# Kernel tuning notes

Measured on AMD Instinct MI355X. Metric: run time of the kernel, lower is better.

## Reference

```python
import jax, jax.numpy as jnp
import numpy as np

B, N, M, D, K = 64, 1024, 1024, 200, 80


def setup_inputs() -> dict:
    key = jax.random.key(0)
    ks = jax.random.split(key, 7)
    return {
        "sentence_rep": jax.random.normal(ks[0], (B, N, D), dtype=jnp.float32),
        "comment_rep": jax.random.normal(ks[1], (B, M, D), dtype=jnp.float32),
        "Wl": jax.random.uniform(ks[2], (D, D), dtype=jnp.float32),
        "Wc": jax.random.uniform(ks[3], (K, D), dtype=jnp.float32),
        "Ws": jax.random.uniform(ks[4], (K, D), dtype=jnp.float32),
        "whs": jax.random.uniform(ks[5], (1, K), dtype=jnp.float32),
        "whc": jax.random.uniform(ks[6], (1, K), dtype=jnp.float32),
    }


def reference(sentence_rep, comment_rep, Wl, Wc, Ws, whs, whc):
    # affinity: L[b,m,n] = tanh((comment @ Wl) @ sent^T)
    L = jnp.tanh(jnp.einsum("bmd,de,bne->bmn", comment_rep, Wl, sentence_rep))
    # projected reps: Ws @ sent^T -> [B,K,N]; Wc @ comment^T -> [B,K,M]
    WsS = jnp.einsum("kd,bnd->bkn", Ws, sentence_rep)
    WcC = jnp.einsum("kd,bmd->bkm", Wc, comment_rep)
    Hs = jnp.tanh(WsS + jnp.einsum("bkm,bmn->bkn", WcC, L))  # [B,K,N]
    Hc = jnp.tanh(WcC + jnp.einsum("bkn,bmn->bkm", WsS, L))  # [B,K,M]
    # NOTE: original uses F.softmax with no dim on a 3D tensor -> legacy dim=0 (batch axis)
    As = jax.nn.softmax(jnp.einsum("ok,bkn->bon", whs, Hs), axis=0)  # [B,1,N]
    Ac = jax.nn.softmax(jnp.einsum("ok,bkm->bom", whc, Hc), axis=0)  # [B,1,M]
    co_s = jnp.einsum("bnd,bon->bd", sentence_rep, As)  # [B,D]
    co_c = jnp.einsum("bmd,bom->bd", comment_rep, Ac)   # [B,D]
    return jnp.concatenate([co_s, co_c], axis=1)  # [B, 2D]
```

## Files before the change

### kernel.cpp

```cpp
#include <hip/hip_runtime.h>
#include <cmath>

constexpr int CB = 64;
constexpr int CN = 1024;
constexpr int CM = 1024;
constexpr int CD = 200;
constexpr int CK = 80;

__global__ __launch_bounds__(256) void k_transpose(const float* __restrict__ Wl,
                                                   float* __restrict__ WlT) {
  int idx = blockIdx.x * 256 + threadIdx.x;
  if (idx < CD * CD) {
    int d = idx / CD, e = idx - d * CD;
    WlT[e * CD + d] = Wl[idx];
  }
}

__global__ __launch_bounds__(256) void k_rowrow(
    const float* __restrict__ A, long sA,
    const float* __restrict__ Bm, long sB,
    float* __restrict__ C, long sC, int ldc, int I, int J)
{
  const int bz = blockIdx.z;
  A  += (size_t)bz * sA;
  Bm += (size_t)bz * sB;
  C  += (size_t)bz * sC;
  const int i0 = blockIdx.x * 64, j0 = blockIdx.y * 64;
  __shared__ float As[2][16][68];
  __shared__ float Bs[2][16][68];
  const int tid = threadIdx.x;
  const int tx = tid & 15, ty = tid >> 4;
  const int lr = tid >> 2, ld4 = (tid & 3) << 2;
  float acc[4][4] = {};
  for (int ci = 0; ci < 13; ++ci) {
    const int dc = ci * 16;
    const int buf = ci & 1;
    float4 va = make_float4(0.f, 0.f, 0.f, 0.f), vb = va;
    const int gd = dc + ld4;
    if (gd < CD) {
      const int gi = i0 + lr;
      if (gi < I) va = *(const float4*)(A + (size_t)gi * CD + gd);
      const int gj = j0 + lr;
      if (gj < J) vb = *(const float4*)(Bm + (size_t)gj * CD + gd);
    }
    As[buf][ld4 + 0][lr] = va.x; As[buf][ld4 + 1][lr] = va.y;
    As[buf][ld4 + 2][lr] = va.z; As[buf][ld4 + 3][lr] = va.w;
    Bs[buf][ld4 + 0][lr] = vb.x; Bs[buf][ld4 + 1][lr] = vb.y;
    Bs[buf][ld4 + 2][lr] = vb.z; Bs[buf][ld4 + 3][lr] = vb.w;
    __syncthreads();
    #pragma unroll
    for (int dd = 0; dd < 16; ++dd) {
      float4 av = *(const float4*)&As[buf][dd][ty * 4];
      float4 bv = *(const float4*)&Bs[buf][dd][tx * 4];
      acc[0][0] += av.x * bv.x; acc[0][1] += av.x * bv.y; acc[0][2] += av.x * bv.z; acc[0][3] += av.x * bv.w;
      acc[1][0] += av.y * bv.x; acc[1][1] += av.y * bv.y; acc[1][2] += av.y * bv.z; acc[1][3] += av.y * bv.w;
      acc[2][0] += av.z * bv.x; acc[2][1] += av.z * bv.y; acc[2][2] += av.z * bv.z; acc[2][3] += av.z * bv.w;
      acc[3][0] += av.w * bv.x; acc[3][1] += av.w * bv.y; acc[3][2] += av.w * bv.z; acc[3][3] += av.w * bv.w;
    }
  }
  #pragma unroll
  for (int ri = 0; ri < 4; ++ri) {
    const int gi = i0 + ty * 4 + ri;
    const int gj = j0 + tx * 4;
    if (gi < I && gj < J) {
      float4 v; v.x = acc[ri][0]; v.y = acc[ri][1]; v.z = acc[ri][2]; v.w = acc[ri][3];
      *(float4*)(C + (size_t)gi * ldc + gj) = v;
    }
  }
}

__global__ __launch_bounds__(256) void k_fused(
    const float* __restrict__ Arows,
    const float* __restrict__ Brows,
    const float* __restrict__ W,
    float* __restrict__ Out)
{
  const int bz = blockIdx.y;
  Arows += (size_t)bz * (CM * CD);
  Brows += (size_t)bz * (CM * CD);
  W     += (size_t)bz * (CK * 1024);
  Out   += (size_t)bz * (CK * 1024);
  const int j0 = blockIdx.x * 32;
  __shared__ float As[2][16][68];
  __shared__ float Bs[2][16][36];
  __shared__ float Xs[64][36];
  __shared__ float Wt[64][81];
  const int tid = threadIdx.x;
  const int tx8 = tid & 7, ty2 = tid >> 3;
  const int jt = tid & 15, kt = tid >> 4;
  const int lr = tid >> 2, ld4 = (tid & 3) << 2;
  float tacc[5][2] = {};
  for (int it = 0; it < 16; ++it) {
    const int i0 = it * 64;
    float4 wv[5];
    #pragma unroll
    for (int rp = 0; rp < 5; ++rp) {
      const int idx4 = rp * 256 + tid;
      wv[rp] = *(const float4*)(W + (size_t)(idx4 >> 4) * 1024 + i0 + ((idx4 & 15) << 2));
    }
    float xacc[2][4] = {};
    for (int ci = 0; ci < 13; ++ci) {
      const int dc = ci * 16;
      const int buf = ci & 1;
      float4 va = make_float4(0.f, 0.f, 0.f, 0.f), vb = va;
      const int gd = dc + ld4;
      if (gd < CD) {
        va = *(const float4*)(Arows + (size_t)(i0 + lr) * CD + gd);
        if (tid < 128) vb = *(const float4*)(Brows + (size_t)(j0 + lr) * CD + gd);
      }
      As[buf][ld4 + 0][lr] = va.x; As[buf][ld4 + 1][lr] = va.y;
      As[buf][ld4 + 2][lr] = va.z; As[buf][ld4 + 3][lr] = va.w;
      if (tid < 128) {
        Bs[buf][ld4 + 0][lr] = vb.x; Bs[buf][ld4 + 1][lr] = vb.y;
        Bs[buf][ld4 + 2][lr] = vb.z; Bs[buf][ld4 + 3][lr] = vb.w;
      }
      __syncthreads();
      #pragma unroll
      for (int dd = 0; dd < 16; ++dd) {
        float2 av = *(const float2*)&As[buf][dd][ty2 * 2];
        float4 bv = *(const float4*)&Bs[buf][dd][tx8 * 4];
        xacc[0][0] += av.x * bv.x; xacc[0][1] += av.x * bv.y;
        xacc[0][2] += av.x * bv.z; xacc[0][3] += av.x * bv.w;
        xacc[1][0] += av.y * bv.x; xacc[1][1] += av.y * bv.y;
        xacc[1][2] += av.y * bv.z; xacc[1][3] += av.y * bv.w;
      }
    }
    #pragma unroll
    for (int r = 0; r < 2; ++r) {
      float4 v;
      v.x = tanhf(xacc[r][0]); v.y = tanhf(xacc[r][1]);
      v.z = tanhf(xacc[r][2]); v.w = tanhf(xacc[r][3]);
      *(float4*)&Xs[ty2 * 2 + r][tx8 * 4] = v;
    }
    #pragma unroll
    for (int rp = 0; rp < 5; ++rp) {
      const int idx4 = rp * 256 + tid;
      const int k = idx4 >> 4, i4 = (idx4 & 15) << 2;
      Wt[i4 + 0][k] = wv[rp].x; Wt[i4 + 1][k] = wv[rp].y;
      Wt[i4 + 2][k] = wv[rp].z; Wt[i4 + 3][k] = wv[rp].w;
    }
    __syncthreads();
    #pragma unroll 8
    for (int i = 0; i < 64; ++i) {
      float2 xv = *(const float2*)&Xs[i][jt * 2];
      #pragma unroll
      for (int c = 0; c < 5; ++c) {
        float w = Wt[i][kt * 5 + c];
        tacc[c][0] += w * xv.x;
        tacc[c][1] += w * xv.y;
      }
    }
  }
  #pragma unroll
  for (int c = 0; c < 5; ++c) {
    const int k = kt * 5 + c;
    float2 v; v.x = tacc[c][0]; v.y = tacc[c][1];
    *(float2*)(Out + (size_t)k * 1024 + j0 + jt * 2) = v;
  }
}

__global__ __launch_bounds__(256) void k_logits(
    const float* __restrict__ WsS, const float* __restrict__ T1, const float* __restrict__ whs,
    const float* __restrict__ WcC, const float* __restrict__ T2, const float* __restrict__ whc,
    float* __restrict__ z)
{
  const int side = blockIdx.z, b = blockIdx.y;
  const int n = blockIdx.x * 256 + threadIdx.x;
  const float* P  = side ? WcC : WsS;
  const float* T  = side ? T2 : T1;
  const float* wh = side ? whc : whs;
  const size_t base = (size_t)b * CK * 1024 + n;
  float acc = 0.f;
  #pragma unroll 8
  for (int k = 0; k < CK; ++k)
    acc += wh[k] * tanhf(P[base + (size_t)k * 1024] + T[base + (size_t)k * 1024]);
  z[((size_t)side * CB + b) * 1024 + n] = acc;
}

__global__ __launch_bounds__(256) void k_softmax(const float* __restrict__ z,
                                                 float* __restrict__ a) {
  const int idx = blockIdx.x * 256 + threadIdx.x;
  if (idx >= 2 * 1024) return;
  const int side = idx >> 10, n = idx & 1023;
  const float* zc = z + (size_t)side * CB * 1024 + n;
  float mx = -1e30f;
  for (int b = 0; b < CB; ++b) mx = fmaxf(mx, zc[(size_t)b * 1024]);
  float s = 0.f;
  for (int b = 0; b < CB; ++b) s += expf(zc[(size_t)b * 1024] - mx);
  const float inv = 1.0f / s;
  float* ac = a + (size_t)side * CB * 1024 + n;
  for (int b = 0; b < CB; ++b) ac[(size_t)b * 1024] = expf(zc[(size_t)b * 1024] - mx) * inv;
}

__global__ __launch_bounds__(256) void k_wsum(
    const float* __restrict__ sent, const float* __restrict__ comm,
    const float* __restrict__ a, float* __restrict__ partial)
{
  const int t = blockIdx.x, b = blockIdx.y, side = blockIdx.z;
  const int d = threadIdx.x;
  if (d >= CD) return;
  const float* rep = side ? comm : sent;
  const float* aw = a + ((size_t)side * CB + b) * 1024;
  float acc = 0.f;
  const int n0 = t * 128;
  #pragma unroll 4
  for (int n = n0; n < n0 + 128; ++n)
    acc += rep[((size_t)b * 1024 + n) * CD + d] * aw[n];
  partial[(((size_t)side * CB + b) * 8 + t) * CD + d] = acc;
}

__global__ __launch_bounds__(256) void k_reduce(const float* __restrict__ partial,
                                                float* __restrict__ out) {
  const int idx = blockIdx.x * 256 + threadIdx.x;
  if (idx < CB * 2 * CD) {
    const int b = idx / 400, r = idx % 400;
    const int side = r / CD, d = r - side * CD;
    const float* p = partial + (((size_t)side * CB + b) * 8) * CD + d;
    float s = 0.f;
    #pragma unroll
    for (int t = 0; t < 8; ++t) s += p[t * CD];
    out[idx] = s;
  }
}

extern "C" void kernel_launch(void* const* d_in, const int* in_sizes, int n_in,
                              void* d_out, int out_size, void* d_ws, size_t ws_size,
                              hipStream_t stream) {
  (void)in_sizes; (void)n_in; (void)out_size; (void)ws_size;
  const float* sent = (const float*)d_in[0];
  const float* comm = (const float*)d_in[1];
  const float* Wl   = (const float*)d_in[2];
  const float* Wc   = (const float*)d_in[3];
  const float* Ws   = (const float*)d_in[4];
  const float* whs  = (const float*)d_in[5];
  const float* whc  = (const float*)d_in[6];
  float* out = (float*)d_out;

  float* ws      = (float*)d_ws;
  float* WlT     = ws;
  float* CWl     = WlT + 40000;
  float* WsS     = CWl + 13107200;
  float* WcC     = WsS + 5242880;
  float* T1      = WcC + 5242880;
  float* T2      = T1  + 5242880;
  float* z       = T2  + 5242880;
  float* a       = z   + 131072;
  float* partial = a   + 131072;

  k_transpose<<<dim3(157), 256, 0, stream>>>(Wl, WlT);
  k_rowrow<<<dim3(1024, 4, 1), 256, 0, stream>>>(comm, 0L, WlT, 0L,
                                                 CWl, 0L, CD, CB * CM, CD);
  k_rowrow<<<dim3(2, 16, CB), 256, 0, stream>>>(Ws, 0L, sent, (long)CN * CD,
                                                WsS, (long)CK * 1024, 1024, CK, CN);
  k_rowrow<<<dim3(2, 16, CB), 256, 0, stream>>>(Wc, 0L, comm, (long)CM * CD,
                                                WcC, (long)CK * 1024, 1024, CK, CM);
  k_fused<<<dim3(32, CB), 256, 0, stream>>>(CWl, sent, WcC, T1);
  k_fused<<<dim3(32, CB), 256, 0, stream>>>(sent, CWl, WsS, T2);
  k_logits<<<dim3(4, CB, 2), 256, 0, stream>>>(WsS, T1, whs, WcC, T2, whc, z);
  k_softmax<<<dim3(8), 256, 0, stream>>>(z, a);
  k_wsum<<<dim3(8, CB, 2), 256, 0, stream>>>(sent, comm, a, partial);
  k_reduce<<<dim3(100), 256, 0, stream>>>(partial, out);
}
```

Before: 2.067 ms.

## Port fused affinity kernel to bf16x3 split MFMA with larger column tiles

Replaces the scalar FP32 FMA fused kernel, which computes the affinity tile, applies tanh and multiplies by the projection, with MFMA 16x16x32 bf16 instructions. Each FP32 operand is split into high and low bf16 parts and three products are summed to keep near-FP32 accuracy. The column tile doubles to 64 and the D dimension is processed in 32-wide chunks with register prefetch. This targets the FP32 ALU bound of the dominant kernel, at the cost of conversion work, extra LDS traffic and a small accuracy loss from dropping the low×low term.

```diff
diff --git a/kernel.cpp b/kernel.cpp
--- a/kernel.cpp
+++ b/kernel.cpp
@@ -6,6 +6,34 @@
 constexpr int CM = 1024;
 constexpr int CD = 200;
 constexpr int CK = 80;
+
+typedef short  s16x8  __attribute__((ext_vector_type(8)));
+typedef unsigned short u16x8v __attribute__((ext_vector_type(8)));
+typedef unsigned short u16x4v __attribute__((ext_vector_type(4)));
+typedef float  f32x4  __attribute__((ext_vector_type(4)));
+
+#define AOFF(row, byteoff) ((row) * 80  + (byteoff))
+#define TOFF(row, byteoff) ((row) * 144 + (byteoff))
+#define WOFF(row, byteoff) ((row) * 144 + (byteoff))
+
+__device__ inline unsigned short bf16_rtne(float x) {
+  unsigned u = __float_as_uint(x);
+  unsigned r = u + 0x7FFFu + ((u >> 16) & 1u);
+  return (unsigned short)(r >> 16);
+}
+__device__ inline float bf16_to_f(unsigned short h) {
+  return __uint_as_float((unsigned)h << 16);
+}
+__device__ inline void split2(float x, unsigned short& h, unsigned short& l) {
+  h = bf16_rtne(x);
+  l = bf16_rtne(x - bf16_to_f(h));
+}
+__device__ inline float f4e(const float4& v, int e) {
+  return e == 0 ? v.x : e == 1 ? v.y : e == 2 ? v.z : v.w;
+}
+__device__ inline f32x4 mfma16(s16x8 a, s16x8 b, f32x4 c) {
+  return __builtin_amdgcn_mfma_f32_16x16x32_bf16(a, b, c, 0, 0, 0);
+}
 
 __global__ __launch_bounds__(256) void k_transpose(const float* __restrict__ Wl,
                                                    float* __restrict__ WlT) {
@@ -69,7 +97,7 @@
   }
 }
 
-__global__ __launch_bounds__(256) void k_fused(
+__global__ __launch_bounds__(256, 2) void k_fused_mfma(
     const float* __restrict__ Arows,
     const float* __restrict__ Brows,
     const float* __restrict__ W,
@@ -80,83 +108,159 @@
   Brows += (size_t)bz * (CM * CD);
   W     += (size_t)bz * (CK * 1024);
   Out   += (size_t)bz * (CK * 1024);
-  const int j0 = blockIdx.x * 32;
-  __shared__ float As[2][16][68];
-  __shared__ float Bs[2][16][36];
-  __shared__ float Xs[64][36];
-  __shared__ float Wt[64][81];
+  const int j0 = blockIdx.x * 64;
+
+  __shared__ __align__(16) unsigned short sAh[2560], sAl[2560];
+  __shared__ __align__(16) unsigned short sBh[2560], sBl[2560];
+  __shared__ __align__(16) unsigned short sTh[4608], sTl[4608];
+  __shared__ __align__(16) unsigned short sWh[5760], sWl[5760];
+
   const int tid = threadIdx.x;
-  const int tx8 = tid & 7, ty2 = tid >> 3;
-  const int jt = tid & 15, kt = tid >> 4;
-  const int lr = tid >> 2, ld4 = (tid & 3) << 2;
-  float tacc[5][2] = {};
+  const int lane = tid & 63, wid = tid >> 6;
+  const int l15 = lane & 15, l4 = lane >> 4;
+  const int ti = wid >> 1, tj = wid & 1;
+  const int nc = wid;
+  const int srow = tid & 63, sd8 = (tid >> 6) << 3;
+
+  const float* brow = Brows + (size_t)(j0 + srow) * CD;
+
+  f32x4 tacc[5];
+  #pragma unroll
+  for (int q = 0; q < 5; ++q) tacc[q] = (f32x4){0.f, 0.f, 0.f, 0.f};
+
   for (int it = 0; it < 16; ++it) {
     const int i0 = it * 64;
-    float4 wv[5];
-    #pragma unroll
-    for (int rp = 0; rp < 5; ++rp) {
-      const int idx4 = rp * 256 + tid;
-      wv[rp] = *(const float4*)(W + (size_t)(idx4 >> 4) * 1024 + i0 + ((idx4 & 15) << 2));
-    }
-    float xacc[2][4] = {};
-    for (int ci = 0; ci < 13; ++ci) {
-      const int dc = ci * 16;
-      const int buf = ci & 1;
-      float4 va = make_float4(0.f, 0.f, 0.f, 0.f), vb = va;
-      const int gd = dc + ld4;
-      if (gd < CD) {
-        va = *(const float4*)(Arows + (size_t)(i0 + lr) * CD + gd);
-        if (tid < 128) vb = *(const float4*)(Brows + (size_t)(j0 + lr) * CD + gd);
-      }
-      As[buf][ld4 + 0][lr] = va.x; As[buf][ld4 + 1][lr] = va.y;
-      As[buf][ld4 + 2][lr] = va.z; As[buf][ld4 + 3][lr] = va.w;
-      if (tid < 128) {
-        Bs[buf][ld4 + 0][lr] = vb.x; Bs[buf][ld4 + 1][lr] = vb.y;
-        Bs[buf][ld4 + 2][lr] = vb.z; Bs[buf][ld4 + 3][lr] = vb.w;
+    const float* arow = Arows + (size_t)(i0 + srow) * CD;
+
+    f32x4 xacc[2][2];
+    #pragma unroll
+    for (int ih = 0; ih < 2; ++ih)
+      #pragma unroll
+      for (int jh = 0; jh < 2; ++jh) xacc[ih][jh] = (f32x4){0.f, 0.f, 0.f, 0.f};
+
+    float4 a0, a1, b0, b1;
+    {
+      const int gd = sd8;
+      a0 = *(const float4*)(arow + gd);  a1 = *(const float4*)(arow + gd + 4);
+      b0 = *(const float4*)(brow + gd);  b1 = *(const float4*)(brow + gd + 4);
+    }
+    #pragma unroll 1
+    for (int ci = 0; ci < 7; ++ci) {
+      {
+        u16x8v ah, al, bh, bl;
+        #pragma unroll
+        for (int e = 0; e < 4; ++e) {
+          unsigned short h, l;
+          split2(f4e(a0, e), h, l); ah[e] = h; al[e] = l;
+          split2(f4e(b0, e), h, l); bh[e] = h; bl[e] = l;
+        }
+        #pragma unroll
+        for (int e = 0; e < 4; ++e) {
+          unsigned short h, l;
+          split2(f4e(a1, e), h, l); ah[e + 4] = h; al[e + 4] = l;
+          split2(f4e(b1, e), h, l); bh[e + 4] = h; bl[e + 4] = l;
+        }
+        const int sb = AOFF(srow, sd8 * 2);
+        *(u16x8v*)((char*)sAh + sb) = ah;
+        *(u16x8v*)((char*)sAl + sb) = al;
+        *(u16x8v*)((char*)sBh + sb) = bh;
+        *(u16x8v*)((char*)sBl + sb) = bl;
       }
       __syncthreads();
-      #pragma unroll
-      for (int dd = 0; dd < 16; ++dd) {
-        float2 av = *(const float2*)&As[buf][dd][ty2 * 2];
-        float4 bv = *(const float4*)&Bs[buf][dd][tx8 * 4];
-        xacc[0][0] += av.x * bv.x; xacc[0][1] += av.x * bv.y;
-        xacc[0][2] += av.x * bv.z; xacc[0][3] += av.x * bv.w;
-        xacc[1][0] += av.y * bv.x; xacc[1][1] += av.y * bv.y;
-        xacc[1][2] += av.y * bv.z; xacc[1][3] += av.y * bv.w;
-      }
-    }
-    #pragma unroll
-    for (int r = 0; r < 2; ++r) {
-      float4 v;
-      v.x = tanhf(xacc[r][0]); v.y = tanhf(xacc[r][1]);
-      v.z = tanhf(xacc[r][2]); v.w = tanhf(xacc[r][3]);
-      *(float4*)&Xs[ty2 * 2 + r][tx8 * 4] = v;
-    }
-    #pragma unroll
-    for (int rp = 0; rp < 5; ++rp) {
-      const int idx4 = rp * 256 + tid;
-      const int k = idx4 >> 4, i4 = (idx4 & 15) << 2;
-      Wt[i4 + 0][k] = wv[rp].x; Wt[i4 + 1][k] = wv[rp].y;
-      Wt[i4 + 2][k] = wv[rp].z; Wt[i4 + 3][k] = wv[rp].w;
+      if (ci < 6) {
+        const int gd = (ci + 1) * 32 + sd8;
+        float4 z = make_float4(0.f, 0.f, 0.f, 0.f);
+        a0 = (gd + 4 <= CD) ? *(const float4*)(arow + gd)     : z;
+        a1 = (gd + 8 <= CD) ? *(const float4*)(arow + gd + 4) : z;
+        b0 = (gd + 4 <= CD) ? *(const float4*)(brow + gd)     : z;
+        b1 = (gd + 8 <= CD) ? *(const float4*)(brow + gd + 4) : z;
+      }
+      {
+        s16x8 fA[2][2], fB[2][2];
+        #pragma unroll
+        for (int h = 0; h < 2; ++h) {
+          const int ab = AOFF(ti * 32 + h * 16 + l15, l4 * 16);
+          fA[h][0] = *(const s16x8*)((const char*)sAh + ab);
+          fA[h][1] = *(const s16x8*)((const char*)sAl + ab);
+          const int bb = AOFF(tj * 32 + h * 16 + l15, l4 * 16);
+          fB[h][0] = *(const s16x8*)((const char*)sBh + bb);
+          fB[h][1] = *(const s16x8*)((const char*)sBl + bb);
+        }
+        #pragma unroll
+        for (int ih = 0; ih < 2; ++ih)
+          #pragma unroll
+          for (int jh = 0; jh < 2; ++jh) {
+            xacc[ih][jh] = mfma16(fA[ih][0], fB[jh][0], xacc[ih][jh]);
+            xacc[ih][jh] = mfma16(fA[ih][0], fB[jh][1], xacc[ih][jh]);
+            xacc[ih][jh] = mfma16(fA[ih][1], fB[jh][0], xacc[ih][jh]);
+          }
+      }
+      __syncthreads();
+    }
+
+    #pragma unroll
+    for (int ih = 0; ih < 2; ++ih)
+      #pragma unroll
+      for (int jh = 0; jh < 2; ++jh) {
+        const int n  = tj * 32 + jh * 16 + l15;
+        const int ii = ti * 32 + ih * 16 + l4 * 4;
+        u16x4v th, tl;
+        #pragma unroll
+        for (int r = 0; r < 4; ++r) {
+          float x = tanhf(xacc[ih][jh][r]);
+          unsigned short h, l; split2(x, h, l);
+          th[r] = h; tl[r] = l;
+        }
+        const int tb = TOFF(n, ii * 2);
+        *(u16x4v*)((char*)sTh + tb) = th;
+        *(u16x4v*)((char*)sTl + tb) = tl;
+      }
+
+    for (int u = tid; u < 640; u += 256) {
+      const int k = u >> 3, i8 = (u & 7) << 3;
+      const float* wp = W + (size_t)k * 1024 + i0 + i8;
+      float4 w0 = *(const float4*)wp, w1 = *(const float4*)(wp + 4);
+      u16x8v wh, wl;
+      #pragma unroll
+      for (int e = 0; e < 4; ++e) {
+        unsigned short h, l;
+        split2(f4e(w0, e), h, l); wh[e] = h; wl[e] = l;
+      }
+      #pragma unroll
+      for (int e = 0; e < 4; ++e) {
+        unsigned short h, l;
+        split2(f4e(w1, e), h, l); wh[e + 4] = h; wl[e + 4] = l;
+      }
+      const int wb = WOFF(k, i8 * 2);
+      *(u16x8v*)((char*)sWh + wb) = wh;
+      *(u16x8v*)((char*)sWl + wb) = wl;
     }
     __syncthreads();
-    #pragma unroll 8
-    for (int i = 0; i < 64; ++i) {
-      float2 xv = *(const float2*)&Xs[i][jt * 2];
-      #pragma unroll
-      for (int c = 0; c < 5; ++c) {
-        float w = Wt[i][kt * 5 + c];
-        tacc[c][0] += w * xv.x;
-        tacc[c][1] += w * xv.y;
-      }
-    }
-  }
+
+    #pragma unroll
+    for (int ks = 0; ks < 2; ++ks) {
+      const int tb = TOFF(nc * 16 + l15, ks * 64 + l4 * 16);
+      s16x8 fth = *(const s16x8*)((const char*)sTh + tb);
+      s16x8 ftl = *(const s16x8*)((const char*)sTl + tb);
+      #pragma unroll
+      for (int kr = 0; kr < 5; ++kr) {
+        const int wb = WOFF(kr * 16 + l15, ks * 64 + l4 * 16);
+        s16x8 fwh = *(const s16x8*)((const char*)sWh + wb);
+        s16x8 fwl = *(const s16x8*)((const char*)sWl + wb);
+        tacc[kr] = mfma16(fwh, fth, tacc[kr]);
+        tacc[kr] = mfma16(fwh, ftl, tacc[kr]);
+        tacc[kr] = mfma16(fwl, fth, tacc[kr]);
+      }
+    }
+  }
+
   #pragma unroll
-  for (int c = 0; c < 5; ++c) {
-    const int k = kt * 5 + c;
-    float2 v; v.x = tacc[c][0]; v.y = tacc[c][1];
-    *(float2*)(Out + (size_t)k * 1024 + j0 + jt * 2) = v;
-  }
+  for (int kr = 0; kr < 5; ++kr)
+    #pragma unroll
+    for (int r = 0; r < 4; ++r) {
+      const int k = kr * 16 + l4 * 4 + r;
+      Out[(size_t)k * 1024 + j0 + nc * 16 + l15] = tacc[kr][r];
+    }
 }
 
 __global__ __launch_bounds__(256) void k_logits(
@@ -254,8 +358,8 @@
                                                 WsS, (long)CK * 1024, 1024, CK, CN);
   k_rowrow<<<dim3(2, 16, CB), 256, 0, stream>>>(Wc, 0L, comm, (long)CM * CD,
                                                 WcC, (long)CK * 1024, 1024, CK, CM);
-  k_fused<<<dim3(32, CB), 256, 0, stream>>>(CWl, sent, WcC, T1);
-  k_fused<<<dim3(32, CB), 256, 0, stream>>>(sent, CWl, WsS, T2);
+  k_fused_mfma<<<dim3(16, CB), 256, 0, stream>>>(CWl, sent, WcC, T1);
+  k_fused_mfma<<<dim3(16, CB), 256, 0, stream>>>(sent, CWl, WsS, T2);
   k_logits<<<dim3(4, CB, 2), 256, 0, stream>>>(WsS, T1, whs, WcC, T2, whc, z);
   k_softmax<<<dim3(8), 256, 0, stream>>>(z, a);
   k_wsum<<<dim3(8, CB, 2), 256, 0, stream>>>(sent, comm, a, partial);
```

Result: faster. 1.996 ms (-3.4%).
